# Kernel tuning notes

Measured on AMD Instinct MI355X. Metric: run time of the kernel, lower is better.

## Reference

```python
import jax, jax.numpy as jnp
import numpy as np

N_NODES = 16000
N_EDGES = 256000
DIM = 256
HEADS = 8
DH = DIM // HEADS
BLOCKS = 3
EPS = 1e-5


def _ln_graph(x, g, b):
    # PyG LayerNorm, mode='graph', batch=None: scalar mean/std over ALL elements,
    # then per-channel affine.
    x = x - x.mean()
    x = x / (x.std() + EPS)
    return x * g + b


def _block(x, src, dst, x_edge, inv_dist, p):
    (Wq, bq, Wk, bk, Wv, bv, We, Ws, bs, g1, b1, W1, c1, W2, c2, g2, b2) = p
    # per-edge gather + projections  [E, H, DH]
    q = (x[dst] @ Wq + bq).reshape(N_EDGES, HEADS, DH)
    e = (x_edge @ We).reshape(N_EDGES, HEADS, DH)          # lin_edge (no bias)
    k = (x[src] @ Wk + bk).reshape(N_EDGES, HEADS, DH) + e
    # distance-scaled attention logits [E, H]
    alpha = (q * k).sum(-1) * (inv_dist[:, None] / np.sqrt(DH))
    # segment softmax over destination nodes (PyG softmax, +1e-16 in denom)
    amax = jax.ops.segment_max(alpha, dst, num_segments=N_NODES)
    ex = jnp.exp(alpha - amax[dst])
    denom = jax.ops.segment_sum(ex, dst, num_segments=N_NODES)
    attn = ex / (denom[dst] + 1e-16)
    v = (x[src] @ Wv + bv).reshape(N_EDGES, HEADS, DH) + e
    msg = (v * attn[:, :, None]).reshape(N_EDGES, DIM)      # concat heads
    out = jax.ops.segment_sum(msg, dst, num_segments=N_NODES)
    out = out + x @ Ws + bs                                 # root / skip weight
    x = _ln_graph(x + out, g1, b1)                          # mha residual + norm
    ffn = jnp.maximum(x @ W1 + c1, 0.0) @ W2 + c2           # 2-layer ReLU MLP
    return _ln_graph(x + ffn, g2, b2)


def setup_inputs() -> dict:
    key = jax.random.key(0)
    ks = jax.random.split(key, 16)
    s = 0.05
    B = BLOCKS

    def w(k, shape):
        return jax.random.normal(k, shape, jnp.float32) * s

    return {
        'x': jax.random.normal(ks[0], (N_NODES, DIM), jnp.float32),
        'edge_index': jax.random.randint(ks[1], (2, N_EDGES), 0, N_NODES),
        'x_edge': jax.random.normal(ks[2], (N_EDGES, DIM), jnp.float32),
        'x_dist': jax.random.uniform(ks[3], (N_EDGES,), jnp.float32, 1.0, 5.0),
        'Wq': w(ks[4], (B, DIM, DIM)), 'bq': jnp.zeros((B, DIM), jnp.float32),
        'Wk': w(ks[5], (B, DIM, DIM)), 'bk': jnp.zeros((B, DIM), jnp.float32),
        'Wv': w(ks[6], (B, DIM, DIM)), 'bv': jnp.zeros((B, DIM), jnp.float32),
        'We': w(ks[7], (B, DIM, DIM)),
        'Wskip': w(ks[8], (B, DIM, DIM)), 'bskip': jnp.zeros((B, DIM), jnp.float32),
        'ln1_g': jnp.ones((B, DIM), jnp.float32), 'ln1_b': jnp.zeros((B, DIM), jnp.float32),
        'W1': w(ks[9], (B, DIM, 4 * DIM)), 'bf1': jnp.zeros((B, 4 * DIM), jnp.float32),
        'W2': w(ks[10], (B, 4 * DIM, DIM)), 'bf2': jnp.zeros((B, DIM), jnp.float32),
        'ln2_g': jnp.ones((B, DIM), jnp.float32), 'ln2_b': jnp.zeros((B, DIM), jnp.float32),
    }


def reference(x, edge_index, x_edge, x_dist, Wq, bq, Wk, bk, Wv, bv, We,
              Wskip, bskip, ln1_g, ln1_b, W1, bf1, W2, bf2, ln2_g, ln2_b):
    src, dst = edge_index[0], edge_index[1]  # PyG: x_j = x[src], x_i = x[dst]
    inv_dist = 1.0 / x_dist
    for i in range(BLOCKS):
        p = (Wq[i], bq[i], Wk[i], bk[i], Wv[i], bv[i], We[i], Wskip[i], bskip[i],
             ln1_g[i], ln1_b[i], W1[i], bf1[i], W2[i], bf2[i], ln2_g[i], ln2_b[i])
        x = _block(x, src, dst, x_edge, inv_dist, p)
    return x
```

## Files before the change

kernel.cpp:

```cpp
#include <hip/hip_runtime.h>
#include <hip/hip_bf16.h>
#include <cstddef>

#define N_NODES 16000
#define N_EDGES 256000
#define DIM 256
#define HEADS 8
#define DFF 1024
#define LN_EPS 1e-5f
#define CNT ((float)((size_t)N_NODES * DIM))
#define RSDH 0.17677669529663687f

typedef __attribute__((ext_vector_type(8))) short short8;
typedef __attribute__((ext_vector_type(4))) float floatx4;

__device__ __forceinline__ float bf2f(unsigned int s) {
    return __uint_as_float(s << 16);
}

__device__ __forceinline__ float2 ln_ms(const float* __restrict__ s) {
    float mu = s[0] * (1.0f / CNT);
    float var = s[1] * (1.0f / CNT) - mu * mu;
    float2 r; r.x = mu; r.y = 1.0f / (sqrtf(fmaxf(var, 0.0f)) + LN_EPS);
    return r;
}

__device__ __forceinline__ void async16(const __hip_bfloat16* g, __hip_bfloat16* l) {
    __builtin_amdgcn_global_load_lds(
        (const __attribute__((address_space(1))) void*)g,
        (__attribute__((address_space(3))) void*)l, 16, 0, 0);
}

__device__ __forceinline__ void pack8(__hip_bfloat16* d, float4 a, float4 b) {
    union { short8 f; __hip_bfloat16 h[8]; } u;
    u.h[0] = __float2bfloat16(a.x); u.h[1] = __float2bfloat16(a.y);
    u.h[2] = __float2bfloat16(a.z); u.h[3] = __float2bfloat16(a.w);
    u.h[4] = __float2bfloat16(b.x); u.h[5] = __float2bfloat16(b.y);
    u.h[6] = __float2bfloat16(b.z); u.h[7] = __float2bfloat16(b.w);
    *(short8*)d = u.f;
}

template<int BIAS, int RELU, int RES, int OBF16, int ACVT>
__global__ __launch_bounds__(256) void mgemm_k(
    const void* __restrict__ Ap, const __hip_bfloat16* __restrict__ Bt,
    const float* __restrict__ bias, const float* __restrict__ res,
    void* __restrict__ C, int M, int K, int N,
    const float* __restrict__ lnA_s, const float* __restrict__ lnA_g,
    const float* __restrict__ lnA_b,
    const float* __restrict__ lnR_s, const float* __restrict__ lnR_g,
    const float* __restrict__ lnR_b,
    float* __restrict__ ostats)
{
    __shared__ __hip_bfloat16 As[128 * 32];
    __shared__ __hip_bfloat16 Bs[128 * 32];
    __shared__ float rs[8];
    const int tid = threadIdx.x;
    const int lane = tid & 63, wv = tid >> 6;
    const int wm = (wv & 1) * 64, wn = (wv >> 1) * 64;
    const int row0 = blockIdx.y * 128, col0 = blockIdx.x * 128;
    const int lr = tid >> 2;
    const int lk = (tid & 3) * 8;

    float muA = 0.0f, scA = 1.0f;
    if (ACVT && lnA_s) { float2 t = ln_ms(lnA_s); muA = t.x; scA = t.y; }

    floatx4 acc[4][4];
    const floatx4 zf = {0.f, 0.f, 0.f, 0.f};
    #pragma unroll
    for (int i = 0; i < 4; i++)
        #pragma unroll
        for (int j = 0; j < 4; j++) acc[i][j] = zf;

    const int a_fo = (wm + (lane & 15)) * 32 + (lane >> 4) * 8;
    const int b_fo = (wn + (lane & 15)) * 32 + (lane >> 4) * 8;

    for (int k0 = 0; k0 < K; k0 += 32) {
        if (ACVT) {
            const float* A = (const float*)Ap;
            const float* p0 = A + (size_t)(row0 + lr) * K + k0 + lk;
            const float* p1 = A + (size_t)(row0 + lr + 64) * K + k0 + lk;
            float4 v0 = *(const float4*)(p0);
            float4 v1 = *(const float4*)(p0 + 4);
            float4 w0 = *(const float4*)(p1);
            float4 w1 = *(const float4*)(p1 + 4);
            if (lnA_s) {
                float4 ga = *(const float4*)(lnA_g + k0 + lk);
                float4 gb = *(const float4*)(lnA_g + k0 + lk + 4);
                float4 ba = *(const float4*)(lnA_b + k0 + lk);
                float4 bb = *(const float4*)(lnA_b + k0 + lk + 4);
                v0.x = (v0.x - muA) * scA * ga.x + ba.x;
                v0.y = (v0.y - muA) * scA * ga.y + ba.y;
                v0.z = (v0.z - muA) * scA * ga.z + ba.z;
                v0.w = (v0.w - muA) * scA * ga.w + ba.w;
                v1.x = (v1.x - muA) * scA * gb.x + bb.x;
                v1.y = (v1.y - muA) * scA * gb.y + bb.y;
                v1.z = (v1.z - muA) * scA * gb.z + bb.z;
                v1.w = (v1.w - muA) * scA * gb.w + bb.w;
                w0.x = (w0.x - muA) * scA * ga.x + ba.x;
                w0.y = (w0.y - muA) * scA * ga.y + ba.y;
                w0.z = (w0.z - muA) * scA * ga.z + ba.z;
                w0.w = (w0.w - muA) * scA * ga.w + ba.w;
                w1.x = (w1.x - muA) * scA * gb.x + bb.x;
                w1.y = (w1.y - muA) * scA * gb.y + bb.y;
                w1.z = (w1.z - muA) * scA * gb.z + bb.z;
                w1.w = (w1.w - muA) * scA * gb.w + bb.w;
            }
            pack8(As + tid * 8, v0, v1);
            pack8(As + 2048 + tid * 8, w0, w1);
        } else {
            const __hip_bfloat16* A = (const __hip_bfloat16*)Ap;
            async16(A + (size_t)(row0 + lr) * K + k0 + lk, As + tid * 8);
            async16(A + (size_t)(row0 + lr + 64) * K + k0 + lk, As + 2048 + tid * 8);
        }
        async16(Bt + (size_t)(col0 + lr) * K + k0 + lk, Bs + tid * 8);
        async16(Bt + (size_t)(col0 + lr + 64) * K + k0 + lk, Bs + 2048 + tid * 8);
        __syncthreads();
        short8 a[4], b[4];
        #pragma unroll
        for (int i = 0; i < 4; i++) {
            a[i] = *(const short8*)(As + a_fo + i * 16 * 32);
            b[i] = *(const short8*)(Bs + b_fo + i * 16 * 32);
        }
        #pragma unroll
        for (int i = 0; i < 4; i++)
            #pragma unroll
            for (int j = 0; j < 4; j++)
                acc[i][j] = __builtin_amdgcn_mfma_f32_16x16x32_bf16(a[i], b[j], acc[i][j], 0, 0, 0);
        __syncthreads();
    }
    float muR = 0.0f, scR = 1.0f;
    if (RES && lnR_s) { float2 t = ln_ms(lnR_s); muR = t.x; scR = t.y; }
    const int rbase = row0 + wm + (lane >> 4) * 4;
    const int cbase = col0 + wn + (lane & 15);
    float s1 = 0.0f, s2 = 0.0f;
    #pragma unroll
    for (int j = 0; j < 4; j++) {
        const int c = cbase + j * 16;
        float bb = BIAS ? bias[c] : 0.0f;
        float gr = (RES && lnR_s) ? lnR_g[c] : 1.0f;
        float br = (RES && lnR_s) ? lnR_b[c] : 0.0f;
        #pragma unroll
        for (int i = 0; i < 4; i++) {
            #pragma unroll
            for (int r = 0; r < 4; r++) {
                const int rr = rbase + i * 16 + r;
                float v = acc[i][j][r] + bb;
                if (RELU) v = fmaxf(v, 0.0f);
                if (RES) {
                    float rv = res[(size_t)rr * N + c];
                    if (lnR_s) rv = (rv - muR) * scR * gr + br;
                    v += rv;
                }
                if (ostats) { s1 += v; s2 += v * v; }
                if (OBF16 == 2) {
                    const int cc = c & 255;
                    const int idx = ((cc >> 2) << 3) + (cc & 3) + ((c >> 8) << 2);
                    ((__hip_bfloat16*)C)[(size_t)rr * N + idx] = __float2bfloat16(v);
                } else if (OBF16) {
                    ((__hip_bfloat16*)C)[(size_t)rr * N + c] = __float2bfloat16(v);
                } else {
                    ((float*)C)[(size_t)rr * N + c] = v;
                }
            }
        }
    }
    if (ostats) {
        #pragma unroll
        for (int o = 32; o > 0; o >>= 1) {
            s1 += __shfl_down(s1, o);
            s2 += __shfl_down(s2, o);
        }
        if (lane == 0) { rs[wv] = s1; rs[4 + wv] = s2; }
        __syncthreads();
        if (tid == 0) {
            atomicAdd(&ostats[0], rs[0] + rs[1] + rs[2] + rs[3]);
            atomicAdd(&ostats[1], rs[4] + rs[5] + rs[6] + rs[7]);
        }
    }
}

__global__ __launch_bounds__(256) void tcvt_k(const float* __restrict__ src,
                                              __hip_bfloat16* __restrict__ dst,
                                              int R, int C)
{
    __shared__ float t[32][33];
    const int c0 = blockIdx.x * 32, r0 = blockIdx.y * 32;
    const int tx = threadIdx.x & 31, ty = threadIdx.x >> 5;
    #pragma unroll
    for (int j = 0; j < 32; j += 8)
        t[ty + j][tx] = src[(size_t)(r0 + ty + j) * C + c0 + tx];
    __syncthreads();
    #pragma unroll
    for (int j = 0; j < 32; j += 8)
        dst[(size_t)(c0 + ty + j) * R + r0 + tx] = __float2bfloat16(t[tx][ty + j]);
}

__global__ __launch_bounds__(256) void bcat_k(const float* __restrict__ ba,
                                              const float* __restrict__ bb,
                                              const float* __restrict__ bc,
                                              const float* __restrict__ bd,
                                              float* __restrict__ o)
{
    int t = blockIdx.x * 256 + threadIdx.x;
    float v = (t < 256) ? ba[t] : (t < 512) ? bb[t - 256]
            : (t < 768) ? bc[t - 512] : bd[t - 768];
    o[t] = v;
}

__global__ __launch_bounds__(256) void hist_k(const int* __restrict__ dst, int* __restrict__ deg)
{
    int e = blockIdx.x * blockDim.x + threadIdx.x;
    if (e < N_EDGES) atomicAdd(&deg[dst[e]], 1);
}

__global__ __launch_bounds__(1024) void scan_k(const int* __restrict__ deg,
                                               int* __restrict__ rowptr,
                                               int* __restrict__ cursor)
{
    __shared__ int wsum[16];
    const int t = threadIdx.x;
    const int base = t * 16;
    int local[16];
    int s = 0;
    if (t < 1000) {
        #pragma unroll
        for (int j = 0; j < 16; j++) { local[j] = s; s += deg[base + j]; }
    }
    const int lane = t & 63, w = t >> 6;
    int v = s;
    #pragma unroll
    for (int off = 1; off < 64; off <<= 1) {
        int u = __shfl_up(v, off);
        if (lane >= off) v += u;
    }
    if (lane == 63) wsum[w] = v;
    __syncthreads();
    if (t == 0) {
        int r = 0;
        #pragma unroll
        for (int i = 0; i < 16; i++) { int u = wsum[i]; wsum[i] = r; r += u; }
    }
    __syncthreads();
    const int excl = v - s + wsum[w];
    if (t < 1000) {
        #pragma unroll
        for (int j = 0; j < 16; j++) {
            rowptr[base + j] = excl + local[j];
            cursor[base + j] = excl + local[j];
        }
        if (t == 999) rowptr[16000] = excl + s;
    }
}

__global__ __launch_bounds__(256) void scatter_k(const int* __restrict__ dst,
                                                 const int* __restrict__ src,
                                                 const float* __restrict__ xd,
                                                 int* __restrict__ cursor,
                                                 int* __restrict__ eperm,
                                                 int* __restrict__ srcp,
                                                 float* __restrict__ scale)
{
    int e = blockIdx.x * blockDim.x + threadIdx.x;
    if (e < N_EDGES) {
        int pos = atomicAdd(&cursor[dst[e]], 1);
        eperm[pos] = e;
        srcp[pos] = src[e];
        scale[pos] = RSDH / xd[e];
    }
}

__global__ __launch_bounds__(256) void eprep_k(const float* __restrict__ xe,
                                               const int* __restrict__ eperm,
                                               __hip_bfloat16* __restrict__ xeb)
{
    const int r = blockIdx.x * 4 + (threadIdx.x >> 6);
    const int lane = threadIdx.x & 63;
    const int e = eperm[r];
    float4 v = *(const float4*)(xe + (size_t)e * DIM + lane * 4);
    union { short4 s; __hip_bfloat16 h[4]; } u;
    u.h[0] = __float2bfloat16(v.x); u.h[1] = __float2bfloat16(v.y);
    u.h[2] = __float2bfloat16(v.z); u.h[3] = __float2bfloat16(v.w);
    *(short4*)(xeb + (size_t)r * DIM + lane * 4) = u.s;
}

__global__ __launch_bounds__(256) void node_agg_k(
    const float* __restrict__ qs, const __hip_bfloat16* __restrict__ kvb,
    const __hip_bfloat16* __restrict__ Ep,
    const int* __restrict__ srcp, const float* __restrict__ scale,
    const int* __restrict__ rowptr,
    const float* __restrict__ xsrc, const float* __restrict__ lnx_s,
    const float* __restrict__ lnx_g, const float* __restrict__ lnx_b,
    float* __restrict__ y, float* __restrict__ ostats)
{
    __shared__ float rs[8];
    const int lane = threadIdx.x & 63;
    const int wv = threadIdx.x >> 6;
    const int n = blockIdx.x * 4 + wv;
    const float4 q = *(const float4*)(qs + (size_t)n * 512 + lane * 4);
    float a0 = 0, a1 = 0, a2 = 0, a3 = 0, den = 0;
    const int beg = rowptr[n], end = rowptr[n + 1];
    uint4 kvn = {0, 0, 0, 0}; uint2 ebn = {0, 0}; float scn = 0.0f;
    int spf = 0;
    if (beg < end) {
        const int s0 = srcp[beg];
        spf = (beg + 1 < end) ? srcp[beg + 1] : 0;
        kvn = *(const uint4*)(kvb + (size_t)s0 * 512 + lane * 8);
        ebn = *(const uint2*)(Ep + (size_t)beg * DIM + lane * 4);
        scn = scale[beg];
    }
    for (int i = beg; i < end; i++) {
        const uint4 kv = kvn; const uint2 eb = ebn; const float sc = scn;
        if (i + 1 < end) {
            kvn = *(const uint4*)(kvb + (size_t)spf * 512 + lane * 8);
            ebn = *(const uint2*)(Ep + (size_t)(i + 1) * DIM + lane * 4);
            scn = scale[i + 1];
            spf = (i + 2 < end) ? srcp[i + 2] : 0;
        }
        const float e0 = bf2f(eb.x & 0xffffu), e1 = bf2f(eb.x >> 16);
        const float e2 = bf2f(eb.y & 0xffffu), e3 = bf2f(eb.y >> 16);
        float part = q.x * (bf2f(kv.x & 0xffffu) + e0)
                   + q.y * (bf2f(kv.x >> 16) + e1)
                   + q.z * (bf2f(kv.y & 0xffffu) + e2)
                   + q.w * (bf2f(kv.y >> 16) + e3);
        part += __shfl_xor(part, 1);
        part += __shfl_xor(part, 2);
        part += __shfl_xor(part, 4);
        const float ex = __expf(part * sc);
        den += ex;
        a0 = fmaf(bf2f(kv.z & 0xffffu) + e0, ex, a0);
        a1 = fmaf(bf2f(kv.z >> 16) + e1, ex, a1);
        a2 = fmaf(bf2f(kv.w & 0xffffu) + e2, ex, a2);
        a3 = fmaf(bf2f(kv.w >> 16) + e3, ex, a3);
    }
    const float dn = 1.0f / (den + 1e-16f);
    const size_t o = (size_t)n * DIM + lane * 4;
    float4 xr = *(const float4*)(xsrc + o);
    if (lnx_s) {
        float2 t = ln_ms(lnx_s);
        const float4 g4 = *(const float4*)(lnx_g + lane * 4);
        const float4 b4 = *(const float4*)(lnx_b + lane * 4);
        xr.x = (xr.x - t.x) * t.y * g4.x + b4.x;
        xr.y = (xr.y - t.x) * t.y * g4.y + b4.y;
        xr.z = (xr.z - t.x) * t.y * g4.z + b4.z;
        xr.w = (xr.w - t.x) * t.y * g4.w + b4.w;
    }
    const float4 sr = *(const float4*)(qs + (size_t)n * 512 + 256 + lane * 4);
    float4 out;
    out.x = xr.x + a0 * dn + sr.x;
    out.y = xr.y + a1 * dn + sr.y;
    out.z = xr.z + a2 * dn + sr.z;
    out.w = xr.w + a3 * dn + sr.w;
    *(float4*)(y + o) = out;
    float s1 = out.x + out.y + out.z + out.w;
    float s2 = out.x * out.x + out.y * out.y + out.z * out.z + out.w * out.w;
    #pragma unroll
    for (int of = 32; of > 0; of >>= 1) {
        s1 += __shfl_down(s1, of);
        s2 += __shfl_down(s2, of);
    }
    if (lane == 0) { rs[wv] = s1; rs[4 + wv] = s2; }
    __syncthreads();
    if (threadIdx.x == 0) {
        atomicAdd(&ostats[0], rs[0] + rs[1] + rs[2] + rs[3]);
        atomicAdd(&ostats[1], rs[4] + rs[5] + rs[6] + rs[7]);
    }
}

__global__ __launch_bounds__(256) void apply_k(
    const float* __restrict__ y, const float* __restrict__ stats,
    const float* __restrict__ g, const float* __restrict__ b,
    float* __restrict__ xo)
{
    int idx = blockIdx.x * blockDim.x + threadIdx.x;
    float2 t = ln_ms(stats);
    int cb = (idx & 63) * 4;
    float4 v  = *(const float4*)(y + (size_t)idx * 4);
    float4 gv = *(const float4*)(g + cb);
    float4 bv = *(const float4*)(b + cb);
    float4 o;
    o.x = (v.x - t.x) * t.y * gv.x + bv.x;
    o.y = (v.y - t.x) * t.y * gv.y + bv.y;
    o.z = (v.z - t.x) * t.y * gv.z + bv.z;
    o.w = (v.w - t.x) * t.y * gv.w + bv.w;
    *(float4*)(xo + (size_t)idx * 4) = o;
}

extern "C" void kernel_launch(void* const* d_in, const int* in_sizes, int n_in,
                              void* d_out, int out_size, void* d_ws, size_t ws_size,
                              hipStream_t stream) {
    const float* x_in   = (const float*)d_in[0];
    const int*   ei     = (const int*)d_in[1];
    const int*   src    = ei;
    const int*   dstp   = ei + N_EDGES;
    const float* x_edge = (const float*)d_in[2];
    const float* x_dist = (const float*)d_in[3];
    const float* Wq  = (const float*)d_in[4];
    const float* bq  = (const float*)d_in[5];
    const float* Wk  = (const float*)d_in[6];
    const float* bk  = (const float*)d_in[7];
    const float* Wv  = (const float*)d_in[8];
    const float* bv  = (const float*)d_in[9];
    const float* We  = (const float*)d_in[10];
    const float* Wsk = (const float*)d_in[11];
    const float* bsk = (const float*)d_in[12];
    const float* g1  = (const float*)d_in[13];
    const float* b1  = (const float*)d_in[14];
    const float* W1  = (const float*)d_in[15];
    const float* c1  = (const float*)d_in[16];
    const float* W2  = (const float*)d_in[17];
    const float* c2  = (const float*)d_in[18];
    const float* g2  = (const float*)d_in[19];
    const float* b2  = (const float*)d_in[20];

    char* p = (char*)d_ws;
    float* ybuf = (float*)p; p += (size_t)N_NODES * DIM * sizeof(float);
    float* qsb  = (float*)p; p += (size_t)N_NODES * 512 * sizeof(float);
    __hip_bfloat16* kvb = (__hip_bfloat16*)p; p += (size_t)N_NODES * 512 * 2;
    __hip_bfloat16* hb16 = (__hip_bfloat16*)p; p += (size_t)N_NODES * 1024 * 2;
    __hip_bfloat16* Ep   = (__hip_bfloat16*)p; p += (size_t)N_EDGES * DIM * 2;
    __hip_bfloat16* xeb  = (__hip_bfloat16*)p; p += (size_t)N_EDGES * DIM * 2;
    __hip_bfloat16* WqkvsT = (__hip_bfloat16*)p; p += (size_t)3 * 1024 * 256 * 2;
    __hip_bfloat16* WeT    = (__hip_bfloat16*)p; p += (size_t)3 * 256 * 256 * 2;
    __hip_bfloat16* W1T    = (__hip_bfloat16*)p; p += (size_t)3 * 1024 * 256 * 2;
    __hip_bfloat16* W2T    = (__hip_bfloat16*)p; p += (size_t)3 * 256 * 1024 * 2;
    float* bqkvs = (float*)p; p += (size_t)3 * 1024 * sizeof(float);
    float* stats = (float*)p;  p += 64;
    int* deg     = (int*)p;    p += (size_t)N_NODES * sizeof(int);
    int* rowptr  = (int*)p;    p += (size_t)(N_NODES + 4) * sizeof(int);
    int* cursor  = (int*)p;    p += (size_t)N_NODES * sizeof(int);
    int* eperm   = (int*)p;    p += (size_t)N_EDGES * sizeof(int);
    int* srcp    = (int*)p;    p += (size_t)N_EDGES * sizeof(int);
    float* scale = (float*)p;  p += (size_t)N_EDGES * sizeof(float);

    const dim3 blk(256);

    hipMemsetAsync(deg, 0, (size_t)N_NODES * sizeof(int), stream);
    hipMemsetAsync(stats, 0, 48, stream);
    hist_k<<<N_EDGES / 256, blk, 0, stream>>>(dstp, deg);
    scan_k<<<1, 1024, 0, stream>>>(deg, rowptr, cursor);
    scatter_k<<<N_EDGES / 256, blk, 0, stream>>>(dstp, src, x_dist, cursor, eperm, srcp, scale);
    eprep_k<<<N_EDGES / 4, blk, 0, stream>>>(x_edge, eperm, xeb);

    for (int i = 0; i < 3; i++) {
        const float* wsrc[4] = {Wq, Wsk, Wk, Wv};
        for (int c = 0; c < 4; c++)
            tcvt_k<<<dim3(8, 8), blk, 0, stream>>>(wsrc[c] + (size_t)i * 65536,
                WqkvsT + (size_t)i * 262144 + (size_t)c * 65536, 256, 256);
        tcvt_k<<<dim3(8, 8), blk, 0, stream>>>(We + (size_t)i * 65536,
                WeT + (size_t)i * 65536, 256, 256);
        tcvt_k<<<dim3(32, 8), blk, 0, stream>>>(W1 + (size_t)i * 262144,
                W1T + (size_t)i * 262144, 256, 1024);
        tcvt_k<<<dim3(8, 32), blk, 0, stream>>>(W2 + (size_t)i * 262144,
                W2T + (size_t)i * 262144, 1024, 256);
        bcat_k<<<4, blk, 0, stream>>>(bq + (size_t)i * 256, bsk + (size_t)i * 256,
                bk + (size_t)i * 256, bv + (size_t)i * 256, bqkvs + (size_t)i * 1024);
    }

    for (int i = 0; i < 3; i++) {
        const size_t bo = (size_t)i * DIM;
        const size_t b1o = (size_t)i * DFF;
        float* ln1 = stats + (size_t)i * 4;
        float* ln2 = stats + (size_t)i * 4 + 2;
        const float* pls = (i == 0) ? nullptr : stats + (size_t)(i - 1) * 4 + 2;
        const float* plg = (i == 0) ? nullptr : g2 + (size_t)(i - 1) * 256;
        const float* plb = (i == 0) ? nullptr : b2 + (size_t)(i - 1) * 256;
        const float* xsrc = (i == 0) ? x_in : ybuf;

        mgemm_k<1,0,0,0,1><<<dim3(4, 125), blk, 0, stream>>>(
            xsrc, WqkvsT + (size_t)i * 262144, bqkvs + (size_t)i * 1024, nullptr,
            qsb, N_NODES, DIM, 512, pls, plg, plb, nullptr, nullptr, nullptr, nullptr);
        mgemm_k<1,0,0,2,1><<<dim3(4, 125), blk, 0, stream>>>(
            xsrc, WqkvsT + (size_t)i * 262144 + 131072, bqkvs + (size_t)i * 1024 + 512, nullptr,
            kvb, N_NODES, DIM, 512, pls, plg, plb, nullptr, nullptr, nullptr, nullptr);
        mgemm_k<0,0,0,1,0><<<dim3(2, 2000), blk, 0, stream>>>(
            xeb, WeT + (size_t)i * 65536, nullptr, nullptr,
            Ep, N_EDGES, DIM, DIM, nullptr, nullptr, nullptr, nullptr, nullptr, nullptr, nullptr);
        node_agg_k<<<N_NODES / 4, blk, 0, stream>>>(qsb, kvb, Ep, srcp, scale, rowptr,
                                                    xsrc, pls, plg, plb, ybuf, ln1);
        mgemm_k<1,1,0,1,1><<<dim3(8, 125), blk, 0, stream>>>(
            ybuf, W1T + (size_t)i * 262144, c1 + b1o, nullptr,
            hb16, N_NODES, DIM, DFF, ln1, g1 + bo, b1 + bo, nullptr, nullptr, nullptr, nullptr);
        mgemm_k<1,0,1,0,0><<<dim3(2, 125), blk, 0, stream>>>(
            hb16, W2T + (size_t)i * 262144, c2 + bo, ybuf,
            ybuf, N_NODES, DFF, DIM, nullptr, nullptr, nullptr, ln1, g1 + bo, b1 + bo, ln2);
        if (i == 2)
            apply_k<<<(N_NODES * DIM) / 1024, blk, 0, stream>>>(
                ybuf, ln2, g2 + bo, b2 + bo, (float*)d_out);
    }
}
```

Measured before the change: 1.570 ms.

## Add 64-row GEMM tile for FFN down-proj, unroll edge loop, batch weight prep

Adds a TM template parameter so the FFN second GEMM (N=256) runs with 64-row tiles and 500 blocks instead of 250, giving better CU occupancy on the small-N GEMM. node_agg_k now processes two edges per iteration with two independent accumulator sets and a deeper prefetch, to expose more memory-level parallelism on the gathers. Weight transpose and bias concat launches are batched over blocks via a z grid dimension, which cuts the number of launches. The narrower tile lowers MFMA reuse per loaded B tile.

```diff
diff --git a/kernel.cpp b/kernel.cpp
--- a/kernel.cpp
+++ b/kernel.cpp
@@ -40,7 +40,15 @@
     *(short8*)d = u.f;
 }
 
-template<int BIAS, int RELU, int RES, int OBF16, int ACVT>
+__device__ __forceinline__ float4 lnaff(float4 v, float4 g, float4 b, float mu, float sc) {
+    v.x = (v.x - mu) * sc * g.x + b.x;
+    v.y = (v.y - mu) * sc * g.y + b.y;
+    v.z = (v.z - mu) * sc * g.z + b.z;
+    v.w = (v.w - mu) * sc * g.w + b.w;
+    return v;
+}
+
+template<int BIAS, int RELU, int RES, int OBF16, int ACVT, int TM>
 __global__ __launch_bounds__(256) void mgemm_k(
     const void* __restrict__ Ap, const __hip_bfloat16* __restrict__ Bt,
     const float* __restrict__ bias, const float* __restrict__ res,
@@ -51,13 +59,15 @@
     const float* __restrict__ lnR_b,
     float* __restrict__ ostats)
 {
-    __shared__ __hip_bfloat16 As[128 * 32];
+    __shared__ __hip_bfloat16 As[TM * 32];
     __shared__ __hip_bfloat16 Bs[128 * 32];
     __shared__ float rs[8];
     const int tid = threadIdx.x;
     const int lane = tid & 63, wv = tid >> 6;
-    const int wm = (wv & 1) * 64, wn = (wv >> 1) * 64;
-    const int row0 = blockIdx.y * 128, col0 = blockIdx.x * 128;
+    const int wm = (TM == 128) ? (wv & 1) * 64 : 0;
+    const int wn = (TM == 128) ? (wv >> 1) * 64 : wv * 32;
+    const int NJ = (TM == 128) ? 4 : 2;
+    const int row0 = blockIdx.y * TM, col0 = blockIdx.x * 128;
     const int lr = tid >> 2;
     const int lk = (tid & 3) * 8;
 
@@ -78,53 +88,46 @@
         if (ACVT) {
             const float* A = (const float*)Ap;
             const float* p0 = A + (size_t)(row0 + lr) * K + k0 + lk;
-            const float* p1 = A + (size_t)(row0 + lr + 64) * K + k0 + lk;
             float4 v0 = *(const float4*)(p0);
             float4 v1 = *(const float4*)(p0 + 4);
-            float4 w0 = *(const float4*)(p1);
-            float4 w1 = *(const float4*)(p1 + 4);
             if (lnA_s) {
                 float4 ga = *(const float4*)(lnA_g + k0 + lk);
                 float4 gb = *(const float4*)(lnA_g + k0 + lk + 4);
                 float4 ba = *(const float4*)(lnA_b + k0 + lk);
                 float4 bb = *(const float4*)(lnA_b + k0 + lk + 4);
-                v0.x = (v0.x - muA) * scA * ga.x + ba.x;
-                v0.y = (v0.y - muA) * scA * ga.y + ba.y;
-                v0.z = (v0.z - muA) * scA * ga.z + ba.z;
-                v0.w = (v0.w - muA) * scA * ga.w + ba.w;
-                v1.x = (v1.x - muA) * scA * gb.x + bb.x;
-                v1.y = (v1.y - muA) * scA * gb.y + bb.y;
-                v1.z = (v1.z - muA) * scA * gb.z + bb.z;
-                v1.w = (v1.w - muA) * scA * gb.w + bb.w;
-                w0.x = (w0.x - muA) * scA * ga.x + ba.x;
-                w0.y = (w0.y - muA) * scA * ga.y + ba.y;
-                w0.z = (w0.z - muA) * scA * ga.z + ba.z;
-                w0.w = (w0.w - muA) * scA * ga.w + ba.w;
-                w1.x = (w1.x - muA) * scA * gb.x + bb.x;
-                w1.y = (w1.y - muA) * scA * gb.y + bb.y;
-                w1.z = (w1.z - muA) * scA * gb.z + bb.z;
-                w1.w = (w1.w - muA) * scA * gb.w + bb.w;
+                v0 = lnaff(v0, ga, ba, muA, scA);
+                v1 = lnaff(v1, gb, bb, muA, scA);
+                if (TM == 128) {
+                    const float* p1 = A + (size_t)(row0 + lr + 64) * K + k0 + lk;
+                    float4 w0 = lnaff(*(const float4*)(p1), ga, ba, muA, scA);
+                    float4 w1 = lnaff(*(const float4*)(p1 + 4), gb, bb, muA, scA);
+                    pack8(As + 2048 + tid * 8, w0, w1);
+                }
+            } else if (TM == 128) {
+                const float* p1 = A + (size_t)(row0 + lr + 64) * K + k0 + lk;
+                pack8(As + 2048 + tid * 8, *(const float4*)(p1), *(const float4*)(p1 + 4));
             }
             pack8(As + tid * 8, v0, v1);
-            pack8(As + 2048 + tid * 8, w0, w1);
         } else {
             const __hip_bfloat16* A = (const __hip_bfloat16*)Ap;
             async16(A + (size_t)(row0 + lr) * K + k0 + lk, As + tid * 8);
-            async16(A + (size_t)(row0 + lr + 64) * K + k0 + lk, As + 2048 + tid * 8);
+            if (TM == 128)
+                async16(A + (size_t)(row0 + lr + 64) * K + k0 + lk, As + 2048 + tid * 8);
         }
         async16(Bt + (size_t)(col0 + lr) * K + k0 + lk, Bs + tid * 8);
         async16(Bt + (size_t)(col0 + lr + 64) * K + k0 + lk, Bs + 2048 + tid * 8);
         __syncthreads();
         short8 a[4], b[4];
         #pragma unroll
-        for (int i = 0; i < 4; i++) {
+        for (int i = 0; i < 4; i++)
             a[i] = *(const short8*)(As + a_fo + i * 16 * 32);
-            b[i] = *(const short8*)(Bs + b_fo + i * 16 * 32);
-        }
+        #pragma unroll
+        for (int j = 0; j < NJ; j++)
+            b[j] = *(const short8*)(Bs + b_fo + j * 16 * 32);
         #pragma unroll
         for (int i = 0; i < 4; i++)
             #pragma unroll
-            for (int j = 0; j < 4; j++)
+            for (int j = 0; j < NJ; j++)
                 acc[i][j] = __builtin_amdgcn_mfma_f32_16x16x32_bf16(a[i], b[j], acc[i][j], 0, 0, 0);
         __syncthreads();
     }
@@ -134,7 +137,7 @@
     const int cbase = col0 + wn + (lane & 15);
     float s1 = 0.0f, s2 = 0.0f;
     #pragma unroll
-    for (int j = 0; j < 4; j++) {
+    for (int j = 0; j < NJ; j++) {
         const int c = cbase + j * 16;
         float bb = BIAS ? bias[c] : 0.0f;
         float gr = (RES && lnR_s) ? lnR_g[c] : 1.0f;
@@ -181,8 +184,10 @@
 
 __global__ __launch_bounds__(256) void tcvt_k(const float* __restrict__ src,
                                               __hip_bfloat16* __restrict__ dst,
-                                              int R, int C)
-{
+                                              int R, int C, int sStride, int dStride)
+{
+    src += (size_t)blockIdx.z * sStride;
+    dst += (size_t)blockIdx.z * dStride;
     __shared__ float t[32][33];
     const int c0 = blockIdx.x * 32, r0 = blockIdx.y * 32;
     const int tx = threadIdx.x & 31, ty = threadIdx.x >> 5;
@@ -201,10 +206,11 @@
                                               const float* __restrict__ bd,
                                               float* __restrict__ o)
 {
+    const int z = blockIdx.y;
     int t = blockIdx.x * 256 + threadIdx.x;
-    float v = (t < 256) ? ba[t] : (t < 512) ? bb[t - 256]
-            : (t < 768) ? bc[t - 512] : bd[t - 768];
-    o[t] = v;
+    float v = (t < 256) ? ba[z * 256 + t] : (t < 512) ? bb[z * 256 + t - 256]
+            : (t < 768) ? bc[z * 256 + t - 512] : bd[z * 256 + t - 768];
+    o[(size_t)z * 1024 + t] = v;
 }
 
 __global__ __launch_bounds__(256) void hist_k(const int* __restrict__ dst, int* __restrict__ deg)
@@ -297,52 +303,97 @@
     const int wv = threadIdx.x >> 6;
     const int n = blockIdx.x * 4 + wv;
     const float4 q = *(const float4*)(qs + (size_t)n * 512 + lane * 4);
-    float a0 = 0, a1 = 0, a2 = 0, a3 = 0, den = 0;
+    float aA0 = 0, aA1 = 0, aA2 = 0, aA3 = 0, denA = 0;
+    float aB0 = 0, aB1 = 0, aB2 = 0, aB3 = 0, denB = 0;
     const int beg = rowptr[n], end = rowptr[n + 1];
-    uint4 kvn = {0, 0, 0, 0}; uint2 ebn = {0, 0}; float scn = 0.0f;
-    int spf = 0;
-    if (beg < end) {
-        const int s0 = srcp[beg];
-        spf = (beg + 1 < end) ? srcp[beg + 1] : 0;
-        kvn = *(const uint4*)(kvb + (size_t)s0 * 512 + lane * 8);
-        ebn = *(const uint2*)(Ep + (size_t)beg * DIM + lane * 4);
-        scn = scale[beg];
-    }
-    for (int i = beg; i < end; i++) {
-        const uint4 kv = kvn; const uint2 eb = ebn; const float sc = scn;
-        if (i + 1 < end) {
-            kvn = *(const uint4*)(kvb + (size_t)spf * 512 + lane * 8);
-            ebn = *(const uint2*)(Ep + (size_t)(i + 1) * DIM + lane * 4);
-            scn = scale[i + 1];
-            spf = (i + 2 < end) ? srcp[i + 2] : 0;
-        }
-        const float e0 = bf2f(eb.x & 0xffffu), e1 = bf2f(eb.x >> 16);
-        const float e2 = bf2f(eb.y & 0xffffu), e3 = bf2f(eb.y >> 16);
-        float part = q.x * (bf2f(kv.x & 0xffffu) + e0)
-                   + q.y * (bf2f(kv.x >> 16) + e1)
-                   + q.z * (bf2f(kv.y & 0xffffu) + e2)
-                   + q.w * (bf2f(kv.y >> 16) + e3);
-        part += __shfl_xor(part, 1);
-        part += __shfl_xor(part, 2);
-        part += __shfl_xor(part, 4);
-        const float ex = __expf(part * sc);
-        den += ex;
-        a0 = fmaf(bf2f(kv.z & 0xffffu) + e0, ex, a0);
-        a1 = fmaf(bf2f(kv.z >> 16) + e1, ex, a1);
-        a2 = fmaf(bf2f(kv.w & 0xffffu) + e2, ex, a2);
-        a3 = fmaf(bf2f(kv.w >> 16) + e3, ex, a3);
-    }
-    const float dn = 1.0f / (den + 1e-16f);
+    int i = beg;
+    int sC = (i + 2 < end) ? srcp[i + 2] : 0;
+    int sD = (i + 3 < end) ? srcp[i + 3] : 0;
+    uint4 kvA = {0, 0, 0, 0}, kvB = {0, 0, 0, 0};
+    uint2 ebA = {0, 0}, ebB = {0, 0};
+    float scA = 0.f, scB = 0.f;
+    if (i < end) {
+        const int sA = srcp[i];
+        kvA = *(const uint4*)(kvb + (size_t)sA * 512 + lane * 8);
+        ebA = *(const uint2*)(Ep + (size_t)i * DIM + lane * 4);
+        scA = scale[i];
+    }
+    if (i + 1 < end) {
+        const int sB = srcp[i + 1];
+        kvB = *(const uint4*)(kvb + (size_t)sB * 512 + lane * 8);
+        ebB = *(const uint2*)(Ep + (size_t)(i + 1) * DIM + lane * 4);
+        scB = scale[i + 1];
+    }
+    while (i + 1 < end) {
+        const uint4 kA = kvA, kB = kvB;
+        const uint2 eA = ebA, eB = ebB;
+        const float cA = scA, cB = scB;
+        if (i + 2 < end) {
+            kvA = *(const uint4*)(kvb + (size_t)sC * 512 + lane * 8);
+            ebA = *(const uint2*)(Ep + (size_t)(i + 2) * DIM + lane * 4);
+            scA = scale[i + 2];
+            sC = (i + 4 < end) ? srcp[i + 4] : 0;
+        }
+        if (i + 3 < end) {
+            kvB = *(const uint4*)(kvb + (size_t)sD * 512 + lane * 8);
+            ebB = *(const uint2*)(Ep + (size_t)(i + 3) * DIM + lane * 4);
+            scB = scale[i + 3];
+            sD = (i + 5 < end) ? srcp[i + 5] : 0;
+        }
+        const float eA0 = bf2f(eA.x & 0xffffu), eA1 = bf2f(eA.x >> 16);
+        const float eA2 = bf2f(eA.y & 0xffffu), eA3 = bf2f(eA.y >> 16);
+        const float eB0 = bf2f(eB.x & 0xffffu), eB1 = bf2f(eB.x >> 16);
+        const float eB2 = bf2f(eB.y & 0xffffu), eB3 = bf2f(eB.y >> 16);
+        float pA = q.x * (bf2f(kA.x & 0xffffu) + eA0)
+                 + q.y * (bf2f(kA.x >> 16) + eA1)
+                 + q.z * (bf2f(kA.y & 0xffffu) + eA2)
+                 + q.w * (bf2f(kA.y >> 16) + eA3);
+        float pB = q.x * (bf2f(kB.x & 0xffffu) + eB0)
+                 + q.y * (bf2f(kB.x >> 16) + eB1)
+                 + q.z * (bf2f(kB.y & 0xffffu) + eB2)
+                 + q.w * (bf2f(kB.y >> 16) + eB3);
+        pA += __shfl_xor(pA, 1); pB += __shfl_xor(pB, 1);
+        pA += __shfl_xor(pA, 2); pB += __shfl_xor(pB, 2);
+        pA += __shfl_xor(pA, 4); pB += __shfl_xor(pB, 4);
+        const float exA = __expf(pA * cA);
+        const float exB = __expf(pB * cB);
+        denA += exA; denB += exB;
+        aA0 = fmaf(bf2f(kA.z & 0xffffu) + eA0, exA, aA0);
+        aA1 = fmaf(bf2f(kA.z >> 16) + eA1, exA, aA1);
+        aA2 = fmaf(bf2f(kA.w & 0xffffu) + eA2, exA, aA2);
+        aA3 = fmaf(bf2f(kA.w >> 16) + eA3, exA, aA3);
+        aB0 = fmaf(bf2f(kB.z & 0xffffu) + eB0, exB, aB0);
+        aB1 = fmaf(bf2f(kB.z >> 16) + eB1, exB, aB1);
+        aB2 = fmaf(bf2f(kB.w & 0xffffu) + eB2, exB, aB2);
+        aB3 = fmaf(bf2f(kB.w >> 16) + eB3, exB, aB3);
+        i += 2;
+    }
+    if (i < end) {
+        const float e0 = bf2f(ebA.x & 0xffffu), e1 = bf2f(ebA.x >> 16);
+        const float e2 = bf2f(ebA.y & 0xffffu), e3 = bf2f(ebA.y >> 16);
+        float pA = q.x * (bf2f(kvA.x & 0xffffu) + e0)
+                 + q.y * (bf2f(kvA.x >> 16) + e1)
+                 + q.z * (bf2f(kvA.y & 0xffffu) + e2)
+                 + q.w * (bf2f(kvA.y >> 16) + e3);
+        pA += __shfl_xor(pA, 1);
+        pA += __shfl_xor(pA, 2);
+        pA += __shfl_xor(pA, 4);
+        const float ex = __expf(pA * scA);
+        denA += ex;
+        aA0 = fmaf(bf2f(kvA.z & 0xffffu) + e0, ex, aA0);
+        aA1 = fmaf(bf2f(kvA.z >> 16) + e1, ex, aA1);
+        aA2 = fmaf(bf2f(kvA.w & 0xffffu) + e2, ex, aA2);
+        aA3 = fmaf(bf2f(kvA.w >> 16) + e3, ex, aA3);
+    }
+    const float dn = 1.0f / (denA + denB + 1e-16f);
+    const float a0 = aA0 + aB0, a1 = aA1 + aB1, a2 = aA2 + aB2, a3 = aA3 + aB3;
     const size_t o = (size_t)n * DIM + lane * 4;
     float4 xr = *(const float4*)(xsrc + o);
     if (lnx_s) {
         float2 t = ln_ms(lnx_s);
         const float4 g4 = *(const float4*)(lnx_g + lane * 4);
         const float4 b4 = *(const float4*)(lnx_b + lane * 4);
-        xr.x = (xr.x - t.x) * t.y * g4.x + b4.x;
-        xr.y = (xr.y - t.x) * t.y * g4.y + b4.y;
-        xr.z = (xr.z - t.x) * t.y * g4.z + b4.z;
-        xr.w = (xr.w - t.x) * t.y * g4.w + b4.w;
+        xr = lnaff(xr, g4, b4, t.x, t.y);
     }
     const float4 sr = *(const float4*)(qs + (size_t)n * 512 + 256 + lane * 4);
     float4 out;
@@ -377,12 +428,7 @@
     float4 v  = *(const float4*)(y + (size_t)idx * 4);
     float4 gv = *(const float4*)(g + cb);
     float4 bv = *(const float4*)(b + cb);
-    float4 o;
-    o.x = (v.x - t.x) * t.y * gv.x + bv.x;
-    o.y = (v.y - t.x) * t.y * gv.y + bv.y;
-    o.z = (v.z - t.x) * t.y * gv.z + bv.z;
-    o.w = (v.w - t.x) * t.y * gv.w + bv.w;
-    *(float4*)(xo + (size_t)idx * 4) = o;
+    *(float4*)(xo + (size_t)idx * 4) = lnaff(v, gv, bv, t.x, t.y);
 }
 
 extern "C" void kernel_launch(void* const* d_in, const int* in_sizes, int n_in,
@@ -441,20 +487,14 @@
     scatter_k<<<N_EDGES / 256, blk, 0, stream>>>(dstp, src, x_dist, cursor, eperm, srcp, scale);
     eprep_k<<<N_EDGES / 4, blk, 0, stream>>>(x_edge, eperm, xeb);
 
-    for (int i = 0; i < 3; i++) {
-        const float* wsrc[4] = {Wq, Wsk, Wk, Wv};
-        for (int c = 0; c < 4; c++)
-            tcvt_k<<<dim3(8, 8), blk, 0, stream>>>(wsrc[c] + (size_t)i * 65536,
-                WqkvsT + (size_t)i * 262144 + (size_t)c * 65536, 256, 256);
-        tcvt_k<<<dim3(8, 8), blk, 0, stream>>>(We + (size_t)i * 65536,
-                WeT + (size_t)i * 65536, 256, 256);
-        tcvt_k<<<dim3(32, 8), blk, 0, stream>>>(W1 + (size_t)i * 262144,
-                W1T + (size_t)i * 262144, 256, 1024);
-        tcvt_k<<<dim3(8, 32), blk, 0, stream>>>(W2 + (size_t)i * 262144,
-                W2T + (size_t)i * 262144, 1024, 256);
-        bcat_k<<<4, blk, 0, stream>>>(bq + (size_t)i * 256, bsk + (size_t)i * 256,
-                bk + (size_t)i * 256, bv + (size_t)i * 256, bqkvs + (size_t)i * 1024);
-    }
+    tcvt_k<<<dim3(8, 8, 3), blk, 0, stream>>>(Wq,  WqkvsT + 0 * 65536, 256, 256, 65536, 262144);
+    tcvt_k<<<dim3(8, 8, 3), blk, 0, stream>>>(Wsk, WqkvsT + 1 * 65536, 256, 256, 65536, 262144);
+    tcvt_k<<<dim3(8, 8, 3), blk, 0, stream>>>(Wk,  WqkvsT + 2 * 65536, 256, 256, 65536, 262144);
+    tcvt_k<<<dim3(8, 8, 3), blk, 0, stream>>>(Wv,  WqkvsT + 3 * 65536, 256, 256, 65536, 262144);
+    tcvt_k<<<dim3(8, 8, 3), blk, 0, stream>>>(We,  WeT, 256, 256, 65536, 65536);
+    tcvt_k<<<dim3(32, 8, 3), blk, 0, stream>>>(W1, W1T, 256, 1024, 262144, 262144);
+    tcvt_k<<<dim3(8, 32, 3), blk, 0, stream>>>(W2, W2T, 1024, 256, 262144, 262144);
+    bcat_k<<<dim3(4, 3), blk, 0, stream>>>(bq, bsk, bk, bv, bqkvs);
 
     for (int i = 0; i < 3; i++) {
         const size_t bo = (size_t)i * DIM;
@@ -466,21 +506,21 @@
         const float* plb = (i == 0) ? nullptr : b2 + (size_t)(i - 1) * 256;
         const float* xsrc = (i == 0) ? x_in : ybuf;
 
-        mgemm_k<1,0,0,0,1><<<dim3(4, 125), blk, 0, stream>>>(
+        mgemm_k<1,0,0,0,1,128><<<dim3(4, 125), blk, 0, stream>>>(
             xsrc, WqkvsT + (size_t)i * 262144, bqkvs + (size_t)i * 1024, nullptr,
             qsb, N_NODES, DIM, 512, pls, plg, plb, nullptr, nullptr, nullptr, nullptr);
-        mgemm_k<1,0,0,2,1><<<dim3(4, 125), blk, 0, stream>>>(
+        mgemm_k<1,0,0,2,1,128><<<dim3(4, 125), blk, 0, stream>>>(
             xsrc, WqkvsT + (size_t)i * 262144 + 131072, bqkvs + (size_t)i * 1024 + 512, nullptr,
             kvb, N_NODES, DIM, 512, pls, plg, plb, nullptr, nullptr, nullptr, nullptr);
-        mgemm_k<0,0,0,1,0><<<dim3(2, 2000), blk, 0, stream>>>(
+        mgemm_k<0,0,0,1,0,128><<<dim3(2, 2000), blk, 0, stream>>>(
             xeb, WeT + (size_t)i * 65536, nullptr, nullptr,
             Ep, N_EDGES, DIM, DIM, nullptr, nullptr, nullptr, nullptr, nullptr, nullptr, nullptr);
         node_agg_k<<<N_NODES / 4, blk, 0, stream>>>(qsb, kvb, Ep, srcp, scale, rowptr,
                                                     xsrc, pls, plg, plb, ybuf, ln1);
-        mgemm_k<1,1,0,1,1><<<dim3(8, 125), blk, 0, stream>>>(
+        mgemm_k<1,1,0,1,1,128><<<dim3(8, 125), blk, 0, stream>>>(
             ybuf, W1T + (size_t)i * 262144, c1 + b1o, nullptr,
             hb16, N_NODES, DIM, DFF, ln1, g1 + bo, b1 + bo, nullptr, nullptr, nullptr, nullptr);
-        mgemm_k<1,0,1,0,0><<<dim3(2, 125), blk, 0, stream>>>(
+        mgemm_k<1,0,1,0,0,64><<<dim3(2, 250), blk, 0, stream>>>(
             hb16, W2T + (size_t)i * 262144, c2 + bo, ybuf,
             ybuf, N_NODES, DFF, DIM, nullptr, nullptr, nullptr, ln1, g1 + bo, b1 + bo, ln2);
         if (i == 2)
```

Result: faster. 1.517 ms (-3.3%).
